# Kernel optimization log

Hardware: AMD Instinct MI355X
Metric: run time of the kernel (lower is better)

The kernel has to match this reference:

```python
import jax, jax.numpy as jnp
import numpy as np

N_KERNELS = 11

def _kernel_mus(n):
    l = [1.0]
    if n == 1:
        return l
    b = 2.0 / (n - 1)
    l.append(1 - b / 2)
    for i in range(1, n - 1):
        l.append(l[i] - b)
    return l

def _kernel_sigmas(n):
    b = 2.0 / (n - 1)
    l = [0.0001]
    if n == 1:
        return l
    l += [0.5 * b] * (n - 1)
    return l

MU = jnp.asarray(np.array(_kernel_mus(N_KERNELS), dtype=np.float32))      # [K]
SIGMA = jnp.asarray(np.array(_kernel_sigmas(N_KERNELS), dtype=np.float32))  # [K]


def setup_inputs() -> dict:
    key = jax.random.key(0)
    k1, k2, k3, k4 = jax.random.split(key, 4)
    B, Q, D, V, E = 256, 32, 512, 100000, 300
    return {
        "query_tokens": jax.random.randint(k1, (B, Q), 0, V),
        "doc_tokens": jax.random.randint(k2, (B, D), 0, V),
        "emb": jax.random.normal(k3, (V, E), dtype=jnp.float32),
        "fc_w": jax.random.normal(k4, (1, N_KERNELS), dtype=jnp.float32),
        "fc_b": jnp.zeros((1,), dtype=jnp.float32),
    }


def reference(query_tokens, doc_tokens, emb, fc_w, fc_b):
    q_mask = (query_tokens > 0).astype(jnp.float32)  # [B,Q]
    d_mask = (doc_tokens > 0).astype(jnp.float32)    # [B,D]

    qe = emb[query_tokens]  # [B,Q,E]
    de = emb[doc_tokens]    # [B,D,E]

    # Cosine match matrix (CosineMatrixAttention: L2-normalize with tiny eps)
    qn = qe / (jnp.linalg.norm(qe, axis=-1, keepdims=True) + 1e-13)
    dn = de / (jnp.linalg.norm(de, axis=-1, keepdims=True) + 1e-13)
    mm = jnp.einsum("bqe,bde->bqd", qn, dn)  # [B,Q,D]

    mask = q_mask[:, :, None] * d_mask[:, None, :]  # [B,Q,D]
    mm = mm * mask

    # Gaussian RBF kernel pooling: [B,Q,D,K]
    diff = mm[..., None] - MU[None, None, None, :]
    rbf = jnp.exp(-jnp.square(diff) / (2.0 * jnp.square(SIGMA)[None, None, None, :]))
    rbf = rbf * mask[..., None]

    query_kernels = rbf.sum(axis=2)  # [B,Q,K]
    log_qk = jnp.log(jnp.maximum(query_kernels, 1e-10)) * 0.01
    # NOTE: original code computes a masked version but (bug) sums the UNMASKED
    # log_query_kernels; we faithfully replicate that.
    kernels = log_qk.sum(axis=1)  # [B,K]

    score = kernels @ fc_w.T + fc_b  # [B,1]
    return score
```

## Files before the change

### kernel.cpp

```cpp
#include <hip/hip_runtime.h>
#include <hip/hip_bf16.h>
#include <math.h>


#define NB 256
#define NQ 32
#define ND 512
#define NE 300
#define LROW 328
#define SPLITS 2
#define DPB 256
#define CHUNK 32
#define NCHUNK 8
#define NT 512
#define NK 11
#define QK_SZ (NQ * NK)

typedef __bf16 bf16x8 __attribute__((ext_vector_type(8)));
typedef __bf16 bf16x4 __attribute__((ext_vector_type(4)));
typedef float f32x4 __attribute__((ext_vector_type(4)));

__global__ __launch_bounds__(NT, 4) void knrm_main(
    const int* __restrict__ qtok,
    const int* __restrict__ dtok,
    const float* __restrict__ emb,
    float* __restrict__ partial)
{
  __shared__ __align__(16) __bf16 qlds[NQ][LROW];
  __shared__ __align__(16) __bf16 dlds[2][CHUNK][LROW];
  __shared__ float qscale[NQ];
  __shared__ float dscale[2][CHUNK];
  __shared__ float qkl[QK_SZ];

  const int b    = blockIdx.x >> 1;
  const int sp   = blockIdx.x & 1;
  const int t    = threadIdx.x;
  const int lane = t & 63;
  const int w    = t >> 6;
  const bool producer = (w < 4);

  auto stage = [&](int ch, int buf) {
    const int dr = t >> 3;
    const int dj = t & 7;
    const int td = dtok[b * ND + sp * DPB + ch * CHUNK + dr];
    const float4* rowp = (const float4*)(emb + (size_t)td * NE);

    float4 v[10];
    #pragma unroll
    for (int i = 0; i < 9; ++i) v[i] = rowp[dj + 8 * i];
    v[9] = (dj < 3) ? rowp[dj + 72] : make_float4(0.f, 0.f, 0.f, 0.f);

    float ss = 0.0f;
    #pragma unroll
    for (int i = 0; i < 10; ++i) {
      ss += v[i].x * v[i].x + v[i].y * v[i].y + v[i].z * v[i].z + v[i].w * v[i].w;
      if (i < 9 || dj < 3) {
        bf16x4 h;
        h[0] = (__bf16)v[i].x; h[1] = (__bf16)v[i].y;
        h[2] = (__bf16)v[i].z; h[3] = (__bf16)v[i].w;
        *(bf16x4*)&dlds[buf][dr][4 * (dj + 8 * i)] = h;
      }
    }
    if (dj < 5) { bf16x4 z = {}; *(bf16x4*)&dlds[buf][dr][NE + 4 * dj] = z; }
    ss += __shfl_xor(ss, 1, 8);
    ss += __shfl_xor(ss, 2, 8);
    ss += __shfl_xor(ss, 4, 8);
    if (dj == 0) dscale[buf][dr] = (td > 0) ? 1.0f / (sqrtf(ss) + 1e-13f) : 0.0f;
  };

  if (producer) {
    for (int i = t; i < QK_SZ; i += 256)
      if (i % NK) qkl[i] = 0.0f;
    stage(0, 0);
  } else {
    const int r = (t >> 3) & 31;
    const int j = t & 7;
    const int tq = qtok[b * NQ + r];
    const float4* rowp = (const float4*)(emb + (size_t)tq * NE);

    float4 qv[10];
    #pragma unroll
    for (int i = 0; i < 9; ++i) qv[i] = rowp[j + 8 * i];
    qv[9] = (j < 3) ? rowp[j + 72] : make_float4(0.f, 0.f, 0.f, 0.f);

    float ss = 0.0f;
    #pragma unroll
    for (int i = 0; i < 10; ++i) {
      ss += qv[i].x * qv[i].x + qv[i].y * qv[i].y + qv[i].z * qv[i].z + qv[i].w * qv[i].w;
      if (i < 9 || j < 3) {
        bf16x4 h;
        h[0] = (__bf16)qv[i].x; h[1] = (__bf16)qv[i].y;
        h[2] = (__bf16)qv[i].z; h[3] = (__bf16)qv[i].w;
        *(bf16x4*)&qlds[r][4 * (j + 8 * i)] = h;
      }
    }
    if (j < 5) { bf16x4 z = {}; *(bf16x4*)&qlds[r][NE + 4 * j] = z; }
    ss += __shfl_xor(ss, 1, 8);
    ss += __shfl_xor(ss, 2, 8);
    ss += __shfl_xor(ss, 4, 8);
    if (j == 0) qscale[r] = (tq > 0) ? 1.0f / (sqrtf(ss) + 1e-13f) : 0.0f;

    int cnt = 0;
    #pragma unroll 4
    for (int jj = 0; jj < 32; ++jj) {
      int td = dtok[b * ND + sp * DPB + j + 8 * jj];
      cnt += (tq > 0 && td == tq) ? 1 : 0;
    }
    cnt += __shfl_xor(cnt, 1, 8);
    cnt += __shfl_xor(cnt, 2, 8);
    cnt += __shfl_xor(cnt, 4, 8);
    if (j == 0) qkl[r * NK] = (float)cnt;
  }
  __syncthreads();

  const int cw   = w - 4;
  const int mt   = cw >> 1;
  const int nt   = cw & 1;
  const int l15  = lane & 15;
  const int quad = lane >> 4;

  const float muk[10] = {0.9f, 0.7f, 0.5f, 0.3f, 0.1f,
                         -0.1f, -0.3f, -0.5f, -0.7f, -0.9f};
  float rbfacc[4][10];
  #pragma unroll
  for (int r4 = 0; r4 < 4; ++r4)
    #pragma unroll
    for (int k = 0; k < 10; ++k) rbfacc[r4][k] = 0.0f;

  const __bf16* aptr = &qlds[((mt < 0 ? 0 : mt) * 16 + l15) & 31][quad * 8];

  #pragma unroll 1
  for (int ch = 0; ch < NCHUNK; ++ch) {
    if (producer) {
      if (ch + 1 < NCHUNK) stage(ch + 1, (ch + 1) & 1);
    } else {
      const int buf = ch & 1;
      const __bf16* bptr = &dlds[buf][nt * 16 + l15][quad * 8];

      f32x4 acc = {};
      #pragma unroll
      for (int kk = 0; kk < 10; ++kk) {
        bf16x8 av = *(const bf16x8*)(aptr + kk * 32);
        bf16x8 bv = *(const bf16x8*)(bptr + kk * 32);
        acc = __builtin_amdgcn_mfma_f32_16x16x32_bf16(av, bv, acc, 0, 0, 0);
      }

      const float ds = dscale[buf][nt * 16 + l15];
      #pragma unroll
      for (int r4 = 0; r4 < 4; ++r4) {
        const float qs = qscale[mt * 16 + quad * 4 + r4];
        const float s = qs * ds;
        const float mm = (s == 0.0f) ? 1e8f : acc[r4] * s;
        #pragma unroll
        for (int k = 0; k < 10; ++k) {
          float d = mm - muk[k];
          rbfacc[r4][k] += __builtin_amdgcn_exp2f(d * d * -72.13475204444817f);
        }
      }
    }
    __syncthreads();
  }

  if (!producer) {
    #pragma unroll
    for (int r4 = 0; r4 < 4; ++r4)
      #pragma unroll
      for (int k = 0; k < 10; ++k) {
        float vv = rbfacc[r4][k];
        vv += __shfl_xor(vv, 1);
        vv += __shfl_xor(vv, 2);
        vv += __shfl_xor(vv, 4);
        vv += __shfl_xor(vv, 8);
        if (l15 == 0) atomicAdd(&qkl[(mt * 16 + quad * 4 + r4) * NK + k + 1], vv);
      }
  }
  __syncthreads();

  float* pp = partial + ((size_t)b * SPLITS + sp) * QK_SZ;
  for (int i = t; i < QK_SZ; i += NT) pp[i] = qkl[i];
}

__global__ __launch_bounds__(64) void knrm_epi(
    const float* __restrict__ partial,
    const float* __restrict__ fcw,
    const float* __restrict__ fcb,
    float* __restrict__ out)
{
  const int b = blockIdx.x;
  const int lane = threadIdx.x;
  const float* pb = partial + (size_t)b * SPLITS * QK_SZ;
  float acc = 0.0f;
  for (int i = lane; i < QK_SZ; i += 64) {
    float s = pb[i] + pb[i + QK_SZ];
    acc += logf(fmaxf(s, 1e-10f)) * 0.01f * fcw[i % NK];
  }
  #pragma unroll
  for (int off = 1; off < 64; off <<= 1) acc += __shfl_xor(acc, off);
  if (lane == 0) out[b] = acc + fcb[0];
}

extern "C" void kernel_launch(void* const* d_in, const int* in_sizes, int n_in,
                              void* d_out, int out_size, void* d_ws, size_t ws_size,
                              hipStream_t stream) {
  const int* qtok = (const int*)d_in[0];
  const int* dtok = (const int*)d_in[1];
  const float* emb = (const float*)d_in[2];
  const float* fcw = (const float*)d_in[3];
  const float* fcb = (const float*)d_in[4];
  float* out = (float*)d_out;
  float* partial = (float*)d_ws;

  knrm_main<<<NB * SPLITS, NT, 0, stream>>>(qtok, dtok, emb, partial);
  knrm_epi<<<NB, 64, 0, stream>>>(partial, fcw, fcb, out);
}
```

Measured before the change: 194.7 us.

## Prefetch doc embedding rows two chunks ahead and keep query fragments in registers

Splits the producer's staging into separate global-load and convert/write phases, so the loads for chunk ch+2 are in flight while chunk ch+1 is converted and written to LDS. This hides global-memory latency across the barrier-separated loop iterations. Consumer waves also load their query A-fragments and query scales into registers once, instead of rereading them from LDS every chunk. The cost is more registers per thread (the prefetched float4 buffer plus 10 bf16x8 fragments), which could hurt occupancy under launch_bounds(512,4).

```diff
diff --git a/kernel.cpp b/kernel.cpp
--- a/kernel.cpp
+++ b/kernel.cpp
@@ -39,17 +39,21 @@
   const int w    = t >> 6;
   const bool producer = (w < 4);
 
-  auto stage = [&](int ch, int buf) {
-    const int dr = t >> 3;
-    const int dj = t & 7;
-    const int td = dtok[b * ND + sp * DPB + ch * CHUNK + dr];
+  float4 v[10];
+  int td_w = 0;
+  const int dr = t >> 3;
+  const int dj = t & 7;
+  const int tokbase = b * ND + sp * DPB;
+
+  auto issue_loads = [&](int td) {
     const float4* rowp = (const float4*)(emb + (size_t)td * NE);
-
-    float4 v[10];
     #pragma unroll
     for (int i = 0; i < 9; ++i) v[i] = rowp[dj + 8 * i];
     v[9] = (dj < 3) ? rowp[dj + 72] : make_float4(0.f, 0.f, 0.f, 0.f);
-
+    __builtin_amdgcn_sched_barrier(0);
+  };
+
+  auto convert_write = [&](int buf, int td) {
     float ss = 0.0f;
     #pragma unroll
     for (int i = 0; i < 10; ++i) {
@@ -71,7 +75,11 @@
   if (producer) {
     for (int i = t; i < QK_SZ; i += 256)
       if (i % NK) qkl[i] = 0.0f;
-    stage(0, 0);
+    td_w = dtok[tokbase + dr];
+    issue_loads(td_w);
+    convert_write(0, td_w);
+    td_w = dtok[tokbase + CHUNK + dr];
+    issue_loads(td_w);
   } else {
     const int r = (t >> 3) & 31;
     const int j = t & 7;
@@ -122,17 +130,31 @@
   const float muk[10] = {0.9f, 0.7f, 0.5f, 0.3f, 0.1f,
                          -0.1f, -0.3f, -0.5f, -0.7f, -0.9f};
   float rbfacc[4][10];
-  #pragma unroll
-  for (int r4 = 0; r4 < 4; ++r4)
-    #pragma unroll
-    for (int k = 0; k < 10; ++k) rbfacc[r4][k] = 0.0f;
-
-  const __bf16* aptr = &qlds[((mt < 0 ? 0 : mt) * 16 + l15) & 31][quad * 8];
+  bf16x8 av[10];
+  float qsr[4];
+  if (!producer) {
+    const __bf16* ap = &qlds[mt * 16 + l15][quad * 8];
+    #pragma unroll
+    for (int kk = 0; kk < 10; ++kk) av[kk] = *(const bf16x8*)(ap + kk * 32);
+    #pragma unroll
+    for (int r4 = 0; r4 < 4; ++r4) {
+      qsr[r4] = qscale[mt * 16 + quad * 4 + r4];
+      #pragma unroll
+      for (int k = 0; k < 10; ++k) rbfacc[r4][k] = 0.0f;
+    }
+  }
 
   #pragma unroll 1
   for (int ch = 0; ch < NCHUNK; ++ch) {
     if (producer) {
-      if (ch + 1 < NCHUNK) stage(ch + 1, (ch + 1) & 1);
+      if (ch + 1 < NCHUNK) {
+        convert_write((ch + 1) & 1, td_w);
+        if (ch + 2 < NCHUNK) {
+          int td_i = dtok[tokbase + (ch + 2) * CHUNK + dr];
+          issue_loads(td_i);
+          td_w = td_i;
+        }
+      }
     } else {
       const int buf = ch & 1;
       const __bf16* bptr = &dlds[buf][nt * 16 + l15][quad * 8];
@@ -140,16 +162,14 @@
       f32x4 acc = {};
       #pragma unroll
       for (int kk = 0; kk < 10; ++kk) {
-        bf16x8 av = *(const bf16x8*)(aptr + kk * 32);
         bf16x8 bv = *(const bf16x8*)(bptr + kk * 32);
-        acc = __builtin_amdgcn_mfma_f32_16x16x32_bf16(av, bv, acc, 0, 0, 0);
+        acc = __builtin_amdgcn_mfma_f32_16x16x32_bf16(av[kk], bv, acc, 0, 0, 0);
       }
 
       const float ds = dscale[buf][nt * 16 + l15];
       #pragma unroll
       for (int r4 = 0; r4 < 4; ++r4) {
-        const float qs = qscale[mt * 16 + quad * 4 + r4];
-        const float s = qs * ds;
+        const float s = qsr[r4] * ds;
         const float mm = (s == 0.0f) ? 1e8f : acc[r4] * s;
         #pragma unroll
         for (int k = 0; k < 10; ++k) {
```

Measured after the change: 262.1 us. 1.35x slower.
